# Performance work log

Hardware: AMD Instinct MI355X
Metric: run time of the kernel (lower is better)

Reference implementation:

```python
import jax, jax.numpy as jnp
import numpy as np

KSIZE = 3
COUT = 128
GC = 4

def _unfold(x, k):
    # x: [B,C,H,W] -> [B,C,k*k,H,W]; zero pad (k-1)//2, stride 1 (matches nn.Unfold ordering)
    B, C, H, W = x.shape
    p = (k - 1) // 2
    xp = jnp.pad(x, ((0, 0), (0, 0), (p, p), (p, p)))
    return jnp.stack([xp[:, :, i:i + H, j:j + W] for i in range(k) for j in range(k)], axis=2)

def _bn(x, g, b, m, v, eps=1e-5):
    # inference-mode BatchNorm along channel axis 1, any rank
    sh = (1, -1) + (1,) * (x.ndim - 2)
    return (x - m.reshape(sh)) * (g / jnp.sqrt(v + eps)).reshape(sh) + b.reshape(sh)

def setup_inputs():
    key = jax.random.key(0)
    ks = jax.random.split(key, 15)
    B, C, H, W = 4, 128, 56, 56
    mid = C // 4
    OG = COUT * GC
    s = 0.05
    return {
        'x': jax.random.normal(ks[0], (B, C, H, W), jnp.float32),
        'Wk': jax.random.normal(ks[1], (C, C), jnp.float32) * s,
        'bn1_g': jax.random.uniform(ks[2], (C,), jnp.float32, 0.5, 1.5),
        'bn1_b': jax.random.normal(ks[3], (C,), jnp.float32) * s,
        'bn1_m': jnp.zeros((C,), jnp.float32),
        'bn1_v': jnp.ones((C,), jnp.float32),
        'W1': jax.random.normal(ks[4], (mid, 2 * C), jnp.float32) * s,
        'b1': jax.random.normal(ks[5], (mid,), jnp.float32) * s,
        'bn2_g': jax.random.uniform(ks[6], (mid,), jnp.float32, 0.5, 1.5),
        'bn2_b': jax.random.normal(ks[7], (mid,), jnp.float32) * s,
        'bn2_m': jnp.zeros((mid,), jnp.float32),
        'bn2_v': jnp.ones((mid,), jnp.float32),
        'W2': jax.random.normal(ks[8], (OG, mid), jnp.float32) * s,
        'b2': jax.random.normal(ks[9], (OG,), jnp.float32) * s,
        'gn_g': jax.random.uniform(ks[10], (OG,), jnp.float32, 0.5, 1.5),
        'gn_b': jax.random.normal(ks[11], (OG,), jnp.float32) * s,
        'Wv': jax.random.normal(ks[12], (OG, C), jnp.float32) * s,
        'bnv_g': jax.random.uniform(ks[13], (OG,), jnp.float32, 0.5, 1.5),
        'bnv_b': jax.random.normal(ks[14], (OG,), jnp.float32) * s,
        'bnv_m': jnp.zeros((OG,), jnp.float32),
        'bnv_v': jnp.ones((OG,), jnp.float32),
    }

def reference(x, Wk, bn1_g, bn1_b, bn1_m, bn1_v, W1, b1, bn2_g, bn2_b, bn2_m, bn2_v,
              W2, b2, gn_g, gn_b, Wv, bnv_g, bnv_b, bnv_m, bnv_v):
    B, C, H, W = x.shape
    k2 = KSIZE * KSIZE
    # emb_K: 1x1 conv (no bias) + BN + ReLU, then local unfold
    ke = jax.nn.relu(_bn(jnp.einsum('bchw,dc->bdhw', x, Wk), bn1_g, bn1_b, bn1_m, bn1_v))
    Kp = _unfold(ke, KSIZE)                        # [B,C,k2,H,W]
    Q = jnp.broadcast_to(x[:, :, None], Kp.shape)  # repeat x over k2 (einops '(c k)')
    QK = jnp.concatenate([Q, Kp], axis=1)          # [B,2C,k2,H,W]
    # MLP: 1x1 convs act pointwise over (k2,H,W)
    h = jax.nn.relu(_bn(jnp.einsum('bcphw,mc->bmphw', QK, W1) + b1.reshape(1, -1, 1, 1, 1),
                        bn2_g, bn2_b, bn2_m, bn2_v))
    a = jnp.einsum('bmphw,om->bophw', h, W2) + b2.reshape(1, -1, 1, 1, 1)  # [B,COUT*GC,k2,H,W]
    a = a.reshape(B, COUT, GC, k2, H, W)
    # GroupNorm: num_groups=COUT -> normalize over (GC, k2, H, W) per (b, out)
    mu = a.mean(axis=(2, 3, 4, 5), keepdims=True)
    var = jnp.mean(jnp.square(a - mu), axis=(2, 3, 4, 5), keepdims=True)
    a = (a - mu) / jnp.sqrt(var + 1e-5)
    a = a * gn_g.reshape(1, COUT, GC, 1, 1, 1) + gn_b.reshape(1, COUT, GC, 1, 1, 1)
    # emb_V: 1x1 conv (no bias) + BN, then local unfold
    v = _bn(jnp.einsum('bchw,oc->bohw', x, Wv), bnv_g, bnv_b, bnv_m, bnv_v)
    V = _unfold(v, KSIZE).reshape(B, COUT, GC, k2, H, W)
    return jnp.sum(a * V, axis=(2, 3))             # [B,COUT,H,W]
```

## Files before the change

### kernel.cpp

```cpp
#include <hip/hip_runtime.h>
#include <hip/hip_bf16.h>

typedef __hip_bfloat16 bf16;
typedef __attribute__((ext_vector_type(8))) short short8;
typedef __attribute__((ext_vector_type(4))) float f32x4;

#define HWP 3136
#define WD 56
#define PW 58
#define PADP 3364
#define CC 128
#define MIDM 32
#define OGN 512
#define NB 4

enum : int {
  OFF_FLAG = 0,
  OFF_W2F  = 4,
  OFF_SC2  = OFF_W2F + OGN*MIDM,
  OFF_SH2  = OFF_SC2 + MIDM,
  OFF_B1F  = OFF_SH2 + MIDM,
  OFF_B2F  = OFF_B1F + MIDM,
  OFF_GNG  = OFF_B2F + OGN,
  OFF_GNB  = OFF_GNG + OGN,
  OFF_GPART= OFF_GNB + OGN,
  OFF_PQ   = OFF_GPART + NB*128*1056,
  OFF_SS1  = OFF_PQ + NB*OGN*2,
  OFF_SSV  = OFF_SS1 + CC*2,
  OFF_WKB  = OFF_SSV + OGN*2,
  OFF_WVB  = OFF_WKB + CC*CC/2,
  OFF_W1AB = OFF_WVB + OGN*CC/2,
  OFF_W1BB = OFF_W1AB + MIDM*CC/2,
  OFF_HQT  = OFF_W1BB + MIDM*CC/2,
  OFF_GKT  = OFF_HQT + NB*HWP*MIDM/2,
  OFF_VT   = OFF_GKT + NB*PADP*MIDM/2,
  OFF_R1   = OFF_VT + NB*PADP*OGN/2,
  OFF_XT   = OFF_R1,
  OFF_HS   = OFF_R1,
  WS_TOTAL = OFF_R1 + NB*9*HWP*MIDM/2
};

__device__ __forceinline__ float b2f(unsigned short u) {
  bf16 h; *(unsigned short*)&h = u; return __bfloat162float(h);
}
__device__ __forceinline__ unsigned short f2b(float f) {
  bf16 h = __float2bfloat16(f); return *(unsigned short*)&h;
}
__device__ __forceinline__ float ldmix(const void* p, size_t i, bool isbf) {
  return isbf ? __bfloat162float(((const bf16*)p)[i]) : ((const float*)p)[i];
}
__device__ __forceinline__ f32x4 mfma16(short8 a, short8 b, f32x4 c) {
  return __builtin_amdgcn_mfma_f32_16x16x32_bf16(a, b, c, 0, 0, 0);
}
__device__ __forceinline__ bool detect_bf(const unsigned short* xr) {
  int cnt = 0;
#pragma unroll
  for (int i = 0; i < 32; i++) {
    short8 v = *(const short8*)(xr + i*8);
#pragma unroll
    for (int j = 0; j < 8; j++) {
      int e = (((unsigned short)v[j]) >> 7) & 0xFF;
      cnt += (e >= 141) ? 1 : 0;
    }
  }
  return cnt < 8;
}

__global__ __launch_bounds__(256) void k_prep(
    const void* __restrict__ x,  const void* __restrict__ Wk,
    const void* __restrict__ bn1_g, const void* __restrict__ bn1_b,
    const void* __restrict__ bn1_m, const void* __restrict__ bn1_v,
    const void* __restrict__ W1, const void* __restrict__ b1,
    const void* __restrict__ bn2_g, const void* __restrict__ bn2_b,
    const void* __restrict__ bn2_m, const void* __restrict__ bn2_v,
    const void* __restrict__ W2, const void* __restrict__ b2,
    const void* __restrict__ gn_g, const void* __restrict__ gn_b,
    const void* __restrict__ Wv,
    const void* __restrict__ bnv_g, const void* __restrict__ bnv_b,
    const void* __restrict__ bnv_m, const void* __restrict__ bnv_v,
    float* __restrict__ ws) {
  __shared__ unsigned short tile[32*130];
  const bool isbf = detect_bf((const unsigned short*)x);
  int blk = blockIdx.x, tid = threadIdx.x;
  if (blk == 0 && tid == 0) ws[OFF_FLAG] = isbf ? 1.f : 0.f;
  int gid = blk*256 + tid, gstride = gridDim.x*256;
  unsigned short* wkb = (unsigned short*)(ws + OFF_WKB);
  unsigned short* wvb = (unsigned short*)(ws + OFF_WVB);
  unsigned short* w1ab = (unsigned short*)(ws + OFF_W1AB);
  unsigned short* w1bb = (unsigned short*)(ws + OFF_W1BB);
  float2* ss1 = (float2*)(ws + OFF_SS1);
  float2* ssv = (float2*)(ws + OFF_SSV);
  for (int i = gid; i < CC*CC; i += gstride) wkb[i] = f2b(ldmix(Wk, i, isbf));
  for (int i = gid; i < OGN*CC; i += gstride) wvb[i] = f2b(ldmix(Wv, i, isbf));
  for (int i = gid; i < MIDM*CC; i += gstride) {
    int m = i / CC, c = i % CC;
    w1ab[i] = f2b(ldmix(W1, (size_t)m*(2*CC) + c, isbf));
    w1bb[i] = f2b(ldmix(W1, (size_t)m*(2*CC) + CC + c, isbf));
  }
  for (int i = gid; i < OGN*MIDM; i += gstride) ws[OFF_W2F + i] = ldmix(W2, i, isbf);
  for (int i = gid; i < CC; i += gstride) {
    float s = ldmix(bn1_g, i, isbf) / sqrtf(ldmix(bn1_v, i, isbf) + 1e-5f);
    ss1[i] = make_float2(s, ldmix(bn1_b, i, isbf) - ldmix(bn1_m, i, isbf) * s);
  }
  for (int i = gid; i < MIDM; i += gstride) {
    float s = ldmix(bn2_g, i, isbf) / sqrtf(ldmix(bn2_v, i, isbf) + 1e-5f);
    ws[OFF_SC2 + i] = s;
    ws[OFF_SH2 + i] = ldmix(bn2_b, i, isbf) - ldmix(bn2_m, i, isbf) * s;
    ws[OFF_B1F + i] = ldmix(b1, i, isbf);
  }
  for (int i = gid; i < OGN; i += gstride) {
    float s = ldmix(bnv_g, i, isbf) / sqrtf(ldmix(bnv_v, i, isbf) + 1e-5f);
    ssv[i] = make_float2(s, ldmix(bnv_b, i, isbf) - ldmix(bnv_m, i, isbf) * s);
    ws[OFF_B2F + i] = ldmix(b2, i, isbf);
    ws[OFF_GNG + i] = ldmix(gn_g, i, isbf);
    ws[OFF_GNB + i] = ldmix(gn_b, i, isbf);
  }
  if (blk < 392) {
    int b = blk / 98, pix0 = (blk % 98)*32;
#pragma unroll
    for (int k = 0; k < 16; k++) {
      int idx = tid + k*256;
      int c = idx >> 5, pl = idx & 31;
      tile[pl*130 + c] = f2b(ldmix(x, ((size_t)b*CC + c)*HWP + pix0 + pl, isbf));
    }
    __syncthreads();
    unsigned short* xt = (unsigned short*)(ws + OFF_XT);
#pragma unroll
    for (int k = 0; k < 16; k++) {
      int idx = tid + k*256;
      int c = idx & 127, pl = idx >> 7;
      xt[((size_t)b*HWP + pix0 + pl)*CC + c] = tile[pl*130 + c];
    }
  } else {
    const int NV = 912*64, NG = NB*PADP*4;
    const short8 z = {0,0,0,0,0,0,0,0};
    unsigned short* vt = (unsigned short*)(ws + OFF_VT);
    unsigned short* gk = (unsigned short*)(ws + OFF_GKT);
    for (int u = (blk-392)*256 + tid; u < NV + NG; u += 28*256) {
      if (u < NV) {
        int bpp = u >> 6, och = u & 63;
        int b = bpp / 228, j = bpp - b*228;
        int pp;
        if (j < 58)       pp = j;
        else if (j < 116) pp = 57*PW + (j - 58);
        else if (j < 172) pp = (j - 116 + 1)*PW;
        else              pp = (j - 172 + 1)*PW + 57;
        *(short8*)(vt + ((size_t)b*PADP + pp)*OGN + och*8) = z;
      } else {
        int u2 = u - NV;
        int b = u2 / (PADP*4), rem = u2 - b*(PADP*4);
        int pp = rem >> 2, mch = rem & 3;
        *(short8*)(gk + ((size_t)b*PADP + pp)*MIDM + mch*8) = z;
      }
    }
  }
}

__global__ __launch_bounds__(256, 4) void k_mid(float* __restrict__ ws) {
  __shared__ unsigned short keL[4][16][136];
  int bid = blockIdx.x, tid = threadIdx.x;
  int w = tid >> 6, lane = tid & 63, q = lane >> 4, l16 = lane & 15;
  if (bid < 196) {
    int b = bid / 49, bx = bid - (bid/49)*49;
    int pix = bx*64 + w*16 + l16;
    const unsigned short* xt = (const unsigned short*)(ws + OFF_XT) + ((size_t)b*HWP + pix)*CC;
    short8 Bx[4];
#pragma unroll
    for (int kk = 0; kk < 4; kk++) Bx[kk] = *(const short8*)(xt + kk*32 + q*8);
    const unsigned short* wkb = (const unsigned short*)(ws + OFF_WKB);
    const float2* ss = (const float2*)(ws + OFF_SS1);
#pragma unroll
    for (int ot = 0; ot < 8; ot++) {
      int drow = ot*16 + l16;
      f32x4 c = {0.f, 0.f, 0.f, 0.f};
#pragma unroll
      for (int kk = 0; kk < 4; kk++)
        c = mfma16(*(const short8*)(wkb + (size_t)drow*CC + kk*32 + q*8), Bx[kk], c);
      int d0 = ot*16 + q*4;
      ushort4 st;
      { float2 s = ss[d0+0]; st.x = f2b(fmaxf(s.x*c[0] + s.y, 0.f)); }
      { float2 s = ss[d0+1]; st.y = f2b(fmaxf(s.x*c[1] + s.y, 0.f)); }
      { float2 s = ss[d0+2]; st.z = f2b(fmaxf(s.x*c[2] + s.y, 0.f)); }
      { float2 s = ss[d0+3]; st.w = f2b(fmaxf(s.x*c[3] + s.y, 0.f)); }
      *(ushort4*)&keL[w][l16][d0] = st;
    }
    __syncthreads();
    short8 Bk[4];
#pragma unroll
    for (int kk = 0; kk < 4; kk++) Bk[kk] = *(const short8*)&keL[w][l16][kk*32 + q*8];
    const unsigned short* w1a = (const unsigned short*)(ws + OFF_W1AB);
    const unsigned short* w1b = (const unsigned short*)(ws + OFF_W1BB);
    int h0 = pix / WD, w0 = pix - h0*WD;
    int pp = (h0+1)*PW + (w0+1);
    unsigned short* hqt = (unsigned short*)(ws + OFF_HQT) + ((size_t)b*HWP + pix)*MIDM;
    unsigned short* gkt = (unsigned short*)(ws + OFF_GKT) + ((size_t)b*PADP + pp)*MIDM;
#pragma unroll
    for (int mt = 0; mt < 2; mt++) {
      int mrow = mt*16 + l16;
      f32x4 ch = {0.f,0.f,0.f,0.f}, cg = {0.f,0.f,0.f,0.f};
#pragma unroll
      for (int kk = 0; kk < 4; kk++) {
        ch = mfma16(*(const short8*)(w1a + (size_t)mrow*CC + kk*32 + q*8), Bx[kk], ch);
        cg = mfma16(*(const short8*)(w1b + (size_t)mrow*CC + kk*32 + q*8), Bk[kk], cg);
      }
      int m0 = mt*16 + q*4;
      ushort4 sh, sg;
      sh.x = f2b(ch[0]); sh.y = f2b(ch[1]); sh.z = f2b(ch[2]); sh.w = f2b(ch[3]);
      sg.x = f2b(cg[0]); sg.y = f2b(cg[1]); sg.z = f2b(cg[2]); sg.w = f2b(cg[3]);
      *(ushort4*)(hqt + m0) = sh;
      *(ushort4*)(gkt + m0) = sg;
    }
  } else {
    int vid = bid - 196;
    int bx = vid % 49, rest = vid / 49;
    int by = rest & 3, b = rest >> 2;
    int pix = bx*64 + w*16 + l16;
    int h0 = pix / WD, w0 = pix - h0*WD;
    int pp = (h0+1)*PW + (w0+1);
    const unsigned short* xt = (const unsigned short*)(ws + OFF_XT) + ((size_t)b*HWP + pix)*CC;
    short8 B[4];
#pragma unroll
    for (int kk = 0; kk < 4; kk++) B[kk] = *(const short8*)(xt + kk*32 + q*8);
    const unsigned short* wvb = (const unsigned short*)(ws + OFF_WVB);
    const float2* ss = (const float2*)(ws + OFF_SSV);
    unsigned short* vt = (unsigned short*)(ws + OFF_VT) + ((size_t)b*PADP + pp)*OGN;
#pragma unroll
    for (int ot = 0; ot < 8; ot++) {
      int orow = by*128 + ot*16 + l16;
      f32x4 c = {0.f, 0.f, 0.f, 0.f};
#pragma unroll
      for (int kk = 0; kk < 4; kk++)
        c = mfma16(*(const short8*)(wvb + (size_t)orow*CC + kk*32 + q*8), B[kk], c);
      int o0 = by*128 + ot*16 + q*4;
      ushort4 st;
      { float2 s = ss[o0+0]; st.x = f2b(s.x*c[0] + s.y); }
      { float2 s = ss[o0+1]; st.y = f2b(s.x*c[1] + s.y); }
      { float2 s = ss[o0+2]; st.z = f2b(s.x*c[2] + s.y); }
      { float2 s = ss[o0+3]; st.w = f2b(s.x*c[3] + s.y); }
      *(ushort4*)(vt + o0) = st;
    }
  }
}

__global__ __launch_bounds__(256) void k_gramh(float* __restrict__ ws) {
  __shared__ unsigned short tileT[32][264];
  int b = blockIdx.y, bk = blockIdx.x;
  int tid = threadIdx.x;
  int w = tid >> 6, lane = tid & 63, q = lane >> 4, l16 = lane & 15;
  const int base = bk * 882;
  const unsigned short* hqt = (const unsigned short*)(ws + OFF_HQT) + (size_t)b*HWP*MIDM;
  const unsigned short* gkp = (const unsigned short*)(ws + OFF_GKT) + (size_t)b*PADP*MIDM;
  unsigned short* hsb = (unsigned short*)(ws + OFF_HS) + (size_t)b*9*HWP*MIDM;
  float sc2[MIDM], bas0[MIDM];
#pragma unroll
  for (int m = 0; m < MIDM; m++) {
    sc2[m] = ws[OFF_SC2 + m];
    bas0[m] = sc2[m]*ws[OFF_B1F + m] + ws[OFF_SH2 + m];
  }
  f32x4 gLL={0,0,0,0}, gLH={0,0,0,0}, gHH={0,0,0,0}, sL={0,0,0,0}, sH={0,0,0,0};
  short8 ones;
#pragma unroll
  for (int j = 0; j < 8; j++) ones[j] = (short)0x3F80;
  for (int t = 0; t < 4; t++) {
    int r = t*256 + tid;
    bool valid = r < 882;
    int R = valid ? (base + r) : 0;
    int p = R / HWP, pix = R - p*HWP;
    int h0 = pix / WD, w0 = pix - h0*WD;
    int npp = (h0 + p/3)*PW + (w0 + p - (p/3)*3);
    const unsigned short* hq = hqt + (size_t)pix*MIDM;
    const unsigned short* gk = gkp + (size_t)npp*MIDM;
    short8 hb[4];
#pragma unroll
    for (int ch = 0; ch < 4; ch++) {
      short8 th = *(const short8*)(hq + ch*8);
      short8 tg = *(const short8*)(gk + ch*8);
      short8 o;
#pragma unroll
      for (int j = 0; j < 8; j++) {
        int m = ch*8 + j;
        float hv = b2f((unsigned short)th[j]) + b2f((unsigned short)tg[j]);
        float v = fmaxf(sc2[m]*hv + bas0[m], 0.f);
        o[j] = valid ? (short)f2b(v) : (short)0;
      }
      hb[ch] = o;
      if (valid) *(short8*)(hsb + (size_t)R*MIDM + ch*8) = o;
#pragma unroll
      for (int j = 0; j < 8; j++) tileT[ch*8 + j][tid] = (unsigned short)o[j];
    }
    __syncthreads();
#pragma unroll
    for (int cc = 0; cc < 2; cc++) {
      int c = w*2 + cc;
      short8 alo = *(const short8*)&tileT[l16][c*32 + q*8];
      short8 ahi = *(const short8*)&tileT[l16+16][c*32 + q*8];
      gLL = mfma16(alo, alo, gLL);
      gLH = mfma16(alo, ahi, gLH);
      gHH = mfma16(ahi, ahi, gHH);
      sL = mfma16(alo, ones, sL);
      sH = mfma16(ahi, ones, sH);
    }
    __syncthreads();
  }
  float* blob = ws + OFF_GPART + ((size_t)((b*32 + bk)*4 + w))*1056;
#pragma unroll
  for (int r = 0; r < 4; r++) {
    int row = q*4 + r;
    blob[row*32 + l16]             = gLL[r];
    blob[row*32 + 16 + l16]        = gLH[r];
    blob[(16 + l16)*32 + row]      = gLH[r];
    blob[(16 + row)*32 + 16 + l16] = gHH[r];
  }
  if (l16 == 0) {
#pragma unroll
    for (int r = 0; r < 4; r++) {
      blob[1024 + q*4 + r]      = sL[r];
      blob[1024 + 16 + q*4 + r] = sH[r];
    }
  }
}

__global__ __launch_bounds__(512) void k_stats(float* __restrict__ ws) {
  __shared__ float Gs[MIDM*MIDM], S1s[MIDM], saS[OGN], sqS[OGN], muS[128], invS[128];
  int b = blockIdx.x, o = threadIdx.x;
  for (int e = o; e < 1056; e += 512) {
    float s = 0.f;
    const float* pb = ws + OFF_GPART + (size_t)b*128*1056 + e;
    for (int p = 0; p < 128; p++) s += pb[(size_t)p*1056];
    if (e < 1024) Gs[e] = s; else S1s[e - 1024] = s;
  }
  __syncthreads();
  float w2[MIDM];
#pragma unroll
  for (int m = 0; m < MIDM; m++) w2[m] = ws[OFF_W2F + o*MIDM + m];
  float dotS = 0.f;
#pragma unroll
  for (int m = 0; m < MIDM; m++) dotS += w2[m] * S1s[m];
  float quad = 0.f;
  for (int a = 0; a < MIDM; a++) {
    float t = 0.f;
#pragma unroll
    for (int c = 0; c < MIDM; c++) t += Gs[a*MIDM + c] * w2[c];
    quad += w2[a] * t;
  }
  float b2o = ws[OFF_B2F + o];
  const float M = 9.f * HWP;
  saS[o] = dotS + b2o * M;
  sqS[o] = quad + 2.f*b2o*dotS + b2o*b2o*M;
  __syncthreads();
  if (o < 128) {
    float sa = saS[4*o] + saS[4*o+1] + saS[4*o+2] + saS[4*o+3];
    float sq = sqS[4*o] + sqS[4*o+1] + sqS[4*o+2] + sqS[4*o+3];
    const float invN = 1.f / (4.f * M);
    float mu = sa * invN;
    float var = sq * invN - mu*mu;
    muS[o] = mu;
    invS[o] = 1.f / sqrtf(var + 1e-5f);
  }
  __syncthreads();
  int co = o >> 2;
  float alpha = ws[OFF_GNG + o] * invS[co];
  ((float2*)(ws + OFF_PQ))[b*OGN + o] =
      make_float2(alpha, alpha*b2o + ws[OFF_GNB + o] - muS[co]*alpha);
}

#define VSTRIDE 136
__global__ __launch_bounds__(256, 3) void k_out(const float* __restrict__ ws,
                                                void* __restrict__ outp) {
  __shared__ unsigned short tileV[192*VSTRIDE];
  int b = blockIdx.z, by = blockIdx.y;
  int tid = threadIdx.x;
  int w = tid >> 6, lane = tid & 63, q = lane >> 4, l16 = lane & 15;
  int pix0 = blockIdx.x*64;
  int h00 = pix0 / WD, w00 = pix0 - h00*WD;
  int wstart = (h00+1)*PW + (w00+1) - (PW+1);
  const unsigned short* vsrc = (const unsigned short*)(ws + OFF_VT)
      + (size_t)b*PADP*OGN + (size_t)by*128;
#pragma unroll
  for (int i = 0; i < 12; i++) {
    int u = i*256 + tid;
    int wp = u >> 4, col = (u & 15)*8;
    short8 val = *(const short8*)(vsrc + (size_t)(wstart + wp)*OGN + col);
    *(short8*)&tileV[wp*VSTRIDE + col] = val;
  }
  int pix = pix0 + w*16 + l16;
  int h0 = pix / WD, w0 = pix - h0*WD;
  int ppl = (h0+1)*PW + (w0+1) - wstart;
  const bool isbf = ws[OFF_FLAG] > 0.5f;
  const float2* pq = (const float2*)(ws + OFF_PQ) + b*OGN;
  short8 A[8];
  f32x4 Qv[8];
#pragma unroll
  for (int ot = 0; ot < 8; ot++) {
    int orow = by*128 + ot*16 + l16;
    float P = pq[orow].x;
    const float* wrow = ws + OFF_W2F + (size_t)orow*MIDM + q*8;
    short8 a;
#pragma unroll
    for (int j = 0; j < 8; j++) a[j] = (short)f2b(P * wrow[j]);
    A[ot] = a;
    int o0 = by*128 + ot*16 + q*4;
    f32x4 qv = { pq[o0+0].y, pq[o0+1].y, pq[o0+2].y, pq[o0+3].y };
    Qv[ot] = qv;
  }
  const unsigned short* hsb = (const unsigned short*)(ws + OFF_HS) + (size_t)b*9*HWP*MIDM;
  float acc[8];
#pragma unroll
  for (int ot = 0; ot < 8; ot++) acc[ot] = 0.f;
  __syncthreads();
  const int doff[9] = {-PW-1, -PW, -PW+1, -1, 0, 1, PW-1, PW, PW+1};
#pragma unroll
  for (int p = 0; p < 9; p++) {
    int lp = ppl + doff[p];
    short8 B = *(const short8*)(hsb + ((size_t)p*HWP + pix)*MIDM + q*8);
    const unsigned short* vrow = &tileV[lp*VSTRIDE];
#pragma unroll
    for (int ot = 0; ot < 8; ot++) {
      f32x4 c = {0.f, 0.f, 0.f, 0.f};
      c = mfma16(A[ot], B, c);
      ushort4 vv = *(const ushort4*)(vrow + ot*16 + q*4);
      acc[ot] += (c[0] + Qv[ot][0])*b2f(vv.x) + (c[1] + Qv[ot][1])*b2f(vv.y)
               + (c[2] + Qv[ot][2])*b2f(vv.z) + (c[3] + Qv[ot][3])*b2f(vv.w);
    }
  }
#pragma unroll
  for (int ot = 0; ot < 8; ot++) {
    int co = by*32 + ot*4 + q;
    size_t oidx = ((size_t)b*128 + co)*HWP + pix;
    if (isbf) ((unsigned short*)outp)[oidx] = f2b(acc[ot]);
    else      ((float*)outp)[oidx] = acc[ot];
  }
}

extern "C" void kernel_launch(void* const* d_in, const int* in_sizes, int n_in,
                              void* d_out, int out_size, void* d_ws, size_t ws_size,
                              hipStream_t stream) {
  float* ws = (float*)d_ws;
  hipLaunchKernelGGL(k_prep, dim3(420), dim3(256), 0, stream,
                     d_in[0], d_in[1], d_in[2], d_in[3], d_in[4], d_in[5],
                     d_in[6], d_in[7], d_in[8], d_in[9], d_in[10], d_in[11],
                     d_in[12], d_in[13], d_in[14], d_in[15], d_in[16],
                     d_in[17], d_in[18], d_in[19], d_in[20], ws);
  hipLaunchKernelGGL(k_mid,  dim3(980),      dim3(256), 0, stream, ws);
  hipLaunchKernelGGL(k_gramh,dim3(32, 4),    dim3(256), 0, stream, ws);
  hipLaunchKernelGGL(k_stats,dim3(4),        dim3(512), 0, stream, ws);
  hipLaunchKernelGGL(k_out,  dim3(49, 4, 4), dim3(256), 0, stream, ws, d_out);
}
```

Baseline: 239.6 us.

## Recompute relu hidden in output kernel from tiled halo instead of materializing

The BN2 scale and bias are folded into the projection epilogue that writes hq and gk, so the gram kernel only adds them and applies relu, and it no longer writes the 9x hidden tensor to global memory. The output kernel now works on 8x8 spatial tiles with a 10x10 halo in shared memory for both V and gk. It recomputes the relu hidden values on the fly rather than reading the stored 9-way hidden buffer. Occupancy is raised to 4 blocks per CU. This removes a large global write and read in exchange for extra conversion and ALU work per tap and a gather-style tile load.

```diff
diff --git a/kernel.cpp b/kernel.cpp
--- a/kernel.cpp
+++ b/kernel.cpp
@@ -19,8 +19,7 @@
   OFF_W2F  = 4,
   OFF_SC2  = OFF_W2F + OGN*MIDM,
   OFF_SH2  = OFF_SC2 + MIDM,
-  OFF_B1F  = OFF_SH2 + MIDM,
-  OFF_B2F  = OFF_B1F + MIDM,
+  OFF_B2F  = OFF_SH2 + MIDM,
   OFF_GNG  = OFF_B2F + OGN,
   OFF_GNB  = OFF_GNG + OGN,
   OFF_GPART= OFF_GNB + OGN,
@@ -34,10 +33,8 @@
   OFF_HQT  = OFF_W1BB + MIDM*CC/2,
   OFF_GKT  = OFF_HQT + NB*HWP*MIDM/2,
   OFF_VT   = OFF_GKT + NB*PADP*MIDM/2,
-  OFF_R1   = OFF_VT + NB*PADP*OGN/2,
-  OFF_XT   = OFF_R1,
-  OFF_HS   = OFF_R1,
-  WS_TOTAL = OFF_R1 + NB*9*HWP*MIDM/2
+  OFF_XT   = OFF_VT + NB*PADP*OGN/2,
+  WS_TOTAL = OFF_XT + NB*HWP*CC/2
 };
 
 __device__ __forceinline__ float b2f(unsigned short u) {
@@ -105,8 +102,8 @@
   for (int i = gid; i < MIDM; i += gstride) {
     float s = ldmix(bn2_g, i, isbf) / sqrtf(ldmix(bn2_v, i, isbf) + 1e-5f);
     ws[OFF_SC2 + i] = s;
-    ws[OFF_SH2 + i] = ldmix(bn2_b, i, isbf) - ldmix(bn2_m, i, isbf) * s;
-    ws[OFF_B1F + i] = ldmix(b1, i, isbf);
+    ws[OFF_SH2 + i] = s*ldmix(b1, i, isbf)
+                    + ldmix(bn2_b, i, isbf) - ldmix(bn2_m, i, isbf)*s;
   }
   for (int i = gid; i < OGN; i += gstride) {
     float s = ldmix(bnv_g, i, isbf) / sqrtf(ldmix(bnv_v, i, isbf) + 1e-5f);
@@ -205,8 +202,14 @@
       }
       int m0 = mt*16 + q*4;
       ushort4 sh, sg;
-      sh.x = f2b(ch[0]); sh.y = f2b(ch[1]); sh.z = f2b(ch[2]); sh.w = f2b(ch[3]);
-      sg.x = f2b(cg[0]); sg.y = f2b(cg[1]); sg.z = f2b(cg[2]); sg.w = f2b(cg[3]);
+      sh.x = f2b(ws[OFF_SC2+m0+0]*ch[0] + ws[OFF_SH2+m0+0]);
+      sh.y = f2b(ws[OFF_SC2+m0+1]*ch[1] + ws[OFF_SH2+m0+1]);
+      sh.z = f2b(ws[OFF_SC2+m0+2]*ch[2] + ws[OFF_SH2+m0+2]);
+      sh.w = f2b(ws[OFF_SC2+m0+3]*ch[3] + ws[OFF_SH2+m0+3]);
+      sg.x = f2b(ws[OFF_SC2+m0+0]*cg[0]);
+      sg.y = f2b(ws[OFF_SC2+m0+1]*cg[1]);
+      sg.z = f2b(ws[OFF_SC2+m0+2]*cg[2]);
+      sg.w = f2b(ws[OFF_SC2+m0+3]*cg[3]);
       *(ushort4*)(hqt + m0) = sh;
       *(ushort4*)(gkt + m0) = sg;
     }
@@ -250,13 +253,6 @@
   const int base = bk * 882;
   const unsigned short* hqt = (const unsigned short*)(ws + OFF_HQT) + (size_t)b*HWP*MIDM;
   const unsigned short* gkp = (const unsigned short*)(ws + OFF_GKT) + (size_t)b*PADP*MIDM;
-  unsigned short* hsb = (unsigned short*)(ws + OFF_HS) + (size_t)b*9*HWP*MIDM;
-  float sc2[MIDM], bas0[MIDM];
-#pragma unroll
-  for (int m = 0; m < MIDM; m++) {
-    sc2[m] = ws[OFF_SC2 + m];
-    bas0[m] = sc2[m]*ws[OFF_B1F + m] + ws[OFF_SH2 + m];
-  }
   f32x4 gLL={0,0,0,0}, gLH={0,0,0,0}, gHH={0,0,0,0}, sL={0,0,0,0}, sH={0,0,0,0};
   short8 ones;
 #pragma unroll
@@ -270,23 +266,15 @@
     int npp = (h0 + p/3)*PW + (w0 + p - (p/3)*3);
     const unsigned short* hq = hqt + (size_t)pix*MIDM;
     const unsigned short* gk = gkp + (size_t)npp*MIDM;
-    short8 hb[4];
 #pragma unroll
     for (int ch = 0; ch < 4; ch++) {
       short8 th = *(const short8*)(hq + ch*8);
       short8 tg = *(const short8*)(gk + ch*8);
-      short8 o;
 #pragma unroll
       for (int j = 0; j < 8; j++) {
-        int m = ch*8 + j;
-        float hv = b2f((unsigned short)th[j]) + b2f((unsigned short)tg[j]);
-        float v = fmaxf(sc2[m]*hv + bas0[m], 0.f);
-        o[j] = valid ? (short)f2b(v) : (short)0;
+        float v = fmaxf(b2f((unsigned short)th[j]) + b2f((unsigned short)tg[j]), 0.f);
+        tileT[ch*8 + j][tid] = valid ? f2b(v) : (unsigned short)0;
       }
-      hb[ch] = o;
-      if (valid) *(short8*)(hsb + (size_t)R*MIDM + ch*8) = o;
-#pragma unroll
-      for (int j = 0; j < 8; j++) tileT[ch*8 + j][tid] = (unsigned short)o[j];
     }
     __syncthreads();
 #pragma unroll
@@ -364,28 +352,42 @@
       make_float2(alpha, alpha*b2o + ws[OFF_GNB + o] - muS[co]*alpha);
 }
 
-#define VSTRIDE 136
-__global__ __launch_bounds__(256, 3) void k_out(const float* __restrict__ ws,
+#define VST 136
+#define GST 40
+__global__ __launch_bounds__(256, 4) void k_out(const float* __restrict__ ws,
                                                 void* __restrict__ outp) {
-  __shared__ unsigned short tileV[192*VSTRIDE];
+  __shared__ unsigned short tileV[100*VST];
+  __shared__ unsigned short tileG[100*GST];
   int b = blockIdx.z, by = blockIdx.y;
+  int t = blockIdx.x;
+  int th = t / 7, tw = t - (t/7)*7;
   int tid = threadIdx.x;
   int w = tid >> 6, lane = tid & 63, q = lane >> 4, l16 = lane & 15;
-  int pix0 = blockIdx.x*64;
-  int h00 = pix0 / WD, w00 = pix0 - h00*WD;
-  int wstart = (h00+1)*PW + (w00+1) - (PW+1);
+  int wbase = (th*8)*PW + (tw*8);
   const unsigned short* vsrc = (const unsigned short*)(ws + OFF_VT)
       + (size_t)b*PADP*OGN + (size_t)by*128;
 #pragma unroll
-  for (int i = 0; i < 12; i++) {
+  for (int i = 0; i < 7; i++) {
     int u = i*256 + tid;
-    int wp = u >> 4, col = (u & 15)*8;
-    short8 val = *(const short8*)(vsrc + (size_t)(wstart + wp)*OGN + col);
-    *(short8*)&tileV[wp*VSTRIDE + col] = val;
-  }
-  int pix = pix0 + w*16 + l16;
-  int h0 = pix / WD, w0 = pix - h0*WD;
-  int ppl = (h0+1)*PW + (w0+1) - wstart;
+    if (u < 1600) {
+      int wp = u >> 4, col = (u & 15)*8;
+      int pp = wbase + (wp/10)*PW + (wp - (wp/10)*10);
+      *(short8*)&tileV[wp*VST + col] = *(const short8*)(vsrc + (size_t)pp*OGN + col);
+    }
+  }
+  const unsigned short* gsrc = (const unsigned short*)(ws + OFF_GKT) + (size_t)b*PADP*MIDM;
+#pragma unroll
+  for (int i = 0; i < 2; i++) {
+    int u = i*256 + tid;
+    if (u < 400) {
+      int wp = u >> 2, col = (u & 3)*8;
+      int pp = wbase + (wp/10)*PW + (wp - (wp/10)*10);
+      *(short8*)&tileG[wp*GST + col] = *(const short8*)(gsrc + (size_t)pp*MIDM + col);
+    }
+  }
+  int lr = 2*w + (l16 >> 3), lc = l16 & 7;
+  int pix = (th*8 + lr)*WD + (tw*8 + lc);
+  int lbase = (lr + 1)*10 + (lc + 1);
   const bool isbf = ws[OFF_FLAG] > 0.5f;
   const float2* pq = (const float2*)(ws + OFF_PQ) + b*OGN;
   short8 A[8];
@@ -403,17 +405,26 @@
     f32x4 qv = { pq[o0+0].y, pq[o0+1].y, pq[o0+2].y, pq[o0+3].y };
     Qv[ot] = qv;
   }
-  const unsigned short* hsb = (const unsigned short*)(ws + OFF_HS) + (size_t)b*9*HWP*MIDM;
+  const unsigned short* hq = (const unsigned short*)(ws + OFF_HQT)
+      + ((size_t)b*HWP + pix)*MIDM + q*8;
+  short8 hqv = *(const short8*)hq;
+  float hqf[8];
+#pragma unroll
+  for (int j = 0; j < 8; j++) hqf[j] = b2f((unsigned short)hqv[j]);
   float acc[8];
 #pragma unroll
   for (int ot = 0; ot < 8; ot++) acc[ot] = 0.f;
   __syncthreads();
-  const int doff[9] = {-PW-1, -PW, -PW+1, -1, 0, 1, PW-1, PW, PW+1};
+  const int doff2[9] = {-11, -10, -9, -1, 0, 1, 9, 10, 11};
 #pragma unroll
   for (int p = 0; p < 9; p++) {
-    int lp = ppl + doff[p];
-    short8 B = *(const short8*)(hsb + ((size_t)p*HWP + pix)*MIDM + q*8);
-    const unsigned short* vrow = &tileV[lp*VSTRIDE];
+    int lw = lbase + doff2[p];
+    short8 gv = *(const short8*)&tileG[lw*GST + q*8];
+    short8 B;
+#pragma unroll
+    for (int j = 0; j < 8; j++)
+      B[j] = (short)f2b(fmaxf(hqf[j] + b2f((unsigned short)gv[j]), 0.f));
+    const unsigned short* vrow = &tileV[lw*VST];
 #pragma unroll
     for (int ot = 0; ot < 8; ot++) {
       f32x4 c = {0.f, 0.f, 0.f, 0.f};
```

Result: slower. 298.1 us (+24.4%).
